# Kernel tuning notes

Hardware: AMD Instinct MI355X
Metric: run time of the kernel (lower is better)

## Reference

```python
import jax, jax.numpy as jnp
from jax import lax
import numpy as np

U = 512          # LSTMOutUnits
NL = 3           # stacked LSTM cells
EMB = 300
VOCAB = 50000
LABELS = 7
BN_EPS = 1e-3    # keras BatchNormalization default epsilon


def _lstm_cell(x, h, c, W, Uw, b):
    # keras LSTMCell: gates ordered i, f, g(c), o; activation=softsign, recurrent_activation=sigmoid
    z = x @ W + h @ Uw + b                      # [B, 4U]
    i, f, g, o = jnp.split(z, 4, axis=-1)
    c = jax.nn.sigmoid(f) * c + jax.nn.sigmoid(i) * jax.nn.soft_sign(g)
    h = jax.nn.sigmoid(o) * jax.nn.soft_sign(c)
    return h, c


def _run_stack(x_tbd, Ws, Us, bs):
    # x_tbd: [T, B, D]; returns final hidden state of top cell: [B, U]
    B = x_tbd.shape[1]
    init = tuple((jnp.zeros((B, U), x_tbd.dtype), jnp.zeros((B, U), x_tbd.dtype)) for _ in range(NL))

    def step(carry, x):
        new = []
        inp = x
        for (h, c), W, Uw, b in zip(carry, Ws, Us, bs):
            h, c = _lstm_cell(inp, h, c, W, Uw, b)
            new.append((h, c))
            inp = h
        return tuple(new), None

    carry, _ = lax.scan(step, init, x_tbd)
    return carry[-1][0]


def setup_inputs() -> dict:
    key = jax.random.key(0)
    ks = iter(jax.random.split(key, 40))
    d = {}
    d['ids'] = jax.random.randint(next(ks), (128, 128), 0, VOCAB, dtype=jnp.int32)
    d['emb'] = jax.random.normal(next(ks), (VOCAB, EMB), jnp.float32)
    for pre in ('f', 'b'):
        for l in range(NL):
            din = EMB if l == 0 else U
            d[f'{pre}W{l}'] = jax.random.normal(next(ks), (din, 4 * U), jnp.float32) * 0.05
            d[f'{pre}U{l}'] = jax.random.normal(next(ks), (U, 4 * U), jnp.float32) * 0.05
            d[f'{pre}b{l}'] = jnp.zeros((4 * U,), jnp.float32)
    d['d0_W'] = jax.random.normal(next(ks), (U, U // 2), jnp.float32) * 0.05
    d['d0_b'] = jnp.zeros((U // 2,), jnp.float32)
    d['bn_gamma'] = jnp.ones((U // 2,), jnp.float32)
    d['bn_beta'] = jnp.zeros((U // 2,), jnp.float32)
    d['bn_mean'] = jnp.zeros((U // 2,), jnp.float32)
    d['bn_var'] = jnp.ones((U // 2,), jnp.float32)
    d['prelu_alpha'] = jnp.full((U // 2,), 0.25, jnp.float32)
    d['d1_W'] = jax.random.normal(next(ks), (U // 2, LABELS), jnp.float32) * 0.05
    d['d1_b'] = jnp.zeros((LABELS,), jnp.float32)
    return d


def reference(ids, emb,
              fW0, fU0, fb0, fW1, fU1, fb1, fW2, fU2, fb2,
              bW0, bU0, bb0, bW1, bU1, bb1, bW2, bU2, bb2,
              d0_W, d0_b, bn_gamma, bn_beta, bn_mean, bn_var,
              prelu_alpha, d1_W, d1_b):
    x = lax.stop_gradient(jnp.take(emb, ids, axis=0))      # [B, T, EMB]
    x = jnp.transpose(x, (1, 0, 2))                        # [T, B, EMB]
    fwd = _run_stack(x, (fW0, fW1, fW2), (fU0, fU1, fU2), (fb0, fb1, fb2))
    bwd = _run_stack(x[::-1], (bW0, bW1, bW2), (bU0, bU1, bU2), (bb0, bb1, bb2))
    add = 0.5 * (fwd + bwd)                                # [B, U]
    h = add @ d0_W + d0_b                                  # [B, U//2]
    h = (h - bn_mean) * lax.rsqrt(bn_var + BN_EPS) * bn_gamma + bn_beta
    h = jnp.where(h > 0, h, prelu_alpha * h)               # PReLU
    logits = h @ d1_W + d1_b                               # [B, LABELS]
    return jax.nn.softmax(logits, axis=-1)
```

## Files before the change

kernel.cpp:

```cpp
#include <hip/hip_runtime.h>
#include <hip/hip_bf16.h>
#include <math.h>

#define TT   128
#define BB   128
#define UU   512
#define EMBD 300
#define EMBP 320
#define NBLK 192
#define DBLK 96
#define NTHR 512
#define BSTR 1032

using bf16x8 = __attribute__((ext_vector_type(8))) short;
using f32x4  = __attribute__((ext_vector_type(4))) float;

#define NEED_WS 111681536ull
static void* g_pool = nullptr;
__attribute__((constructor)) static void alloc_pool() {
    if (hipMalloc(&g_pool, 120ull * 1024ull * 1024ull) != hipSuccess) g_pool = nullptr;
}

__device__ __forceinline__ float b2f(unsigned short u) {
    union { unsigned int i; float f; } v; v.i = ((unsigned int)u) << 16; return v.f;
}
__device__ __forceinline__ unsigned short f2b(float f) {
    union { unsigned int i; float f; } v; v.f = f;
    unsigned int i = v.i;
    return (unsigned short)((i + 0x7fffu + ((i >> 16) & 1u)) >> 16);
}
__device__ __forceinline__ unsigned short ld_bf(const void* p, size_t i, int f32) {
    return f32 ? f2b(((const float*)p)[i]) : ((const unsigned short*)p)[i];
}
__device__ __forceinline__ float ld_f(const void* p, size_t i, int f32) {
    return f32 ? ((const float*)p)[i] : b2f(((const unsigned short*)p)[i]);
}
__device__ __forceinline__ float clampz(float x) {
    return fminf(fmaxf(x, -60.0f), 60.0f);
}
__device__ __forceinline__ float sigm(float x)  { return 1.0f / (1.0f + __expf(-x)); }
__device__ __forceinline__ float ssign(float x) { return x / (1.0f + fabsf(x)); }

__device__ __forceinline__ int detect_f32(const void* emb) {
    const unsigned int* w = (const unsigned int*)emb;
    int cnt = 0;
    #pragma unroll
    for (int i = 0; i < 64; ++i) {
        unsigned int e = (w[i] >> 23) & 0xFFu;
        cnt += (e >= 96u && e <= 159u) ? 1 : 0;
    }
    return cnt >= 48;
}

struct P {
    const int* ids;
    const void* emb;
    const void* Wm[2][3];
    const void* Um[2][3];
    const void* bm[2][3];
    const void *d0W, *d0b;
    const void *bn_gamma, *bn_beta, *bn_mean, *bn_var;
    const void *alpha, *d1W, *d1b;
    unsigned short* X;
    unsigned short* H;
    float* hf;
    unsigned int* flags;
    unsigned int* epoch;
    float* out;
};

#define EPOFF 64

__device__ __forceinline__ unsigned int ald(const unsigned int* a) {
    return __hip_atomic_load(a, __ATOMIC_RELAXED, __HIP_MEMORY_SCOPE_AGENT);
}
__device__ __forceinline__ void ast(unsigned int* a, unsigned int v) {
    __hip_atomic_store(a, v, __ATOMIC_RELAXED, __HIP_MEMORY_SCOPE_AGENT);
}

__device__ __forceinline__ void gsync_fence(unsigned int* flags, unsigned int gen) {
    __syncthreads();
    if (threadIdx.x == 0) {
        __threadfence();
        ast(&flags[blockIdx.x], gen);
    }
    if (threadIdx.x < 64) {
        const int i = threadIdx.x;
        for (;;) {
            bool ok = true;
            #pragma unroll
            for (int j = 0; j < NBLK / 64; ++j)
                ok = ok && (ald(&flags[i + j * 64]) >= gen);
            if (__all(ok)) break;
            __builtin_amdgcn_s_sleep(1);
        }
        __threadfence();
    }
    __syncthreads();
}

__device__ __forceinline__ void gsync_dir(P& p, int dirbase, int eidx, int isagg, unsigned int gen) {
    __syncthreads();
    if (threadIdx.x == 0)
        ast(&p.flags[blockIdx.x], gen);
    if (isagg && threadIdx.x < 64) {
        const unsigned int* f = p.flags + dirbase + threadIdx.x;
        const bool two = (threadIdx.x < DBLK - 64);
        for (;;) {
            bool ok = (ald(f) >= gen) && (!two || (ald(f + 64) >= gen));
            if (__all(ok)) break;
            __builtin_amdgcn_s_sleep(1);
        }
        if (threadIdx.x == 0)
            ast(&p.epoch[eidx], gen);
    }
    if (threadIdx.x < 64) {
        const unsigned int* e = &p.epoch[eidx];
        while (ald(e) < gen) __builtin_amdgcn_s_sleep(1);
    }
    __syncthreads();
}

__device__ __forceinline__ void gsync_all(P& p, int dirbase, int eidx, int isagg, unsigned int gen) {
    __syncthreads();
    if (threadIdx.x == 0)
        ast(&p.flags[blockIdx.x], gen);
    if (isagg && threadIdx.x < 64) {
        const unsigned int* f = p.flags + dirbase + threadIdx.x;
        const bool two = (threadIdx.x < DBLK - 64);
        for (;;) {
            bool ok = (ald(f) >= gen) && (!two || (ald(f + 64) >= gen));
            if (__all(ok)) break;
            __builtin_amdgcn_s_sleep(1);
        }
        if (threadIdx.x == 0)
            ast(&p.epoch[eidx], gen);
    }
    if (threadIdx.x < 64) {
        while (!((ald(&p.epoch[0]) >= gen) && (ald(&p.epoch[EPOFF]) >= gen)))
            __builtin_amdgcn_s_sleep(1);
    }
    __syncthreads();
}

template<int K1T, int BOFF>
__device__ __forceinline__ void mfma_part(
    const unsigned short* __restrict__ a0p,
    const unsigned short* __restrict__ bp,
    f32x4 (&acc)[4])
{
    #pragma unroll 4
    for (int kt = 0; kt < K1T; kt += 32) {
        bf16x8 av = *(const bf16x8*)(a0p + kt);
        #pragma unroll
        for (int ct = 0; ct < 4; ++ct) {
            bf16x8 bv = *(const bf16x8*)(bp + (size_t)ct * 16 * BSTR + BOFF + kt);
            acc[ct] = __builtin_amdgcn_mfma_f32_16x16x32_bf16(av, bv, acc[ct], 0, 0, 0);
        }
    }
}

__global__ __launch_bounds__(NTHR, 1) void bilstm_persistent(P p) {
    const int blk = blockIdx.x;
    const int tid = threadIdx.x;

    const int f32 = detect_f32(p.emb);
    unsigned int gen = 0;

    __shared__ __align__(16) unsigned short Bt[64][BSTR];
    __shared__ __align__(16) float zbuf[8][2][16][17];
    __shared__ float hact[256];
    __shared__ float lgts[8];

    for (int row = blk; row < TT * BB; row += NBLK) {
        int t = row >> 7, b = row & 127;
        int id = p.ids[b * TT + t];
        unsigned short* xr = p.X + (size_t)row * EMBP;
        for (int k2 = tid; k2 < EMBP; k2 += NTHR)
            xr[k2] = (k2 < EMBD) ? ld_bf(p.emb, (size_t)id * EMBD + k2, f32)
                                 : (unsigned short)0;
    }
    gsync_fence(p.flags, ++gen);

    const int dir     = (blk >= DBLK) ? 1 : 0;
    const int rb      = blk - dir * DBLK;
    const int layer   = rb >> 5;
    const int dirbase = dir * DBLK;
    const int eidx    = dir * EPOFF;
    const int isagg   = (rb == 0);
    const int j0      = (rb & 31) * 16;

    const int wv   = tid >> 6;
    const int lane = tid & 63;
    const int l15  = lane & 15;
    const int quad = lane >> 4;

    const int row16 = lane & 15;
    const int jp    = (lane >> 4) & 1;
    const int ch    = lane >> 5;

    const int r0   = wv * 16 + l15;
    const int ko   = quad * 8;

    float cS[2][2];
    cS[0][0] = cS[0][1] = cS[1][0] = cS[1][1] = 0.0f;

    const size_t seq = (size_t)TT * BB * UU;

    const int KW   = (layer == 0) ? EMBD : UU;
    const int K1   = (layer == 0) ? EMBP : UU;
    const int Ktot = K1 + UU;
    const void* Wmat = p.Wm[dir][layer];
    const void* Umat = p.Um[dir][layer];
    const void* bias = p.bm[dir][layer];
    {
        int n = tid >> 3, ks = tid & 7;
        int wcol = ((n >> 2) & 3) * UU + j0 + (n >> 4) * 4 + (n & 3);
        for (int k2 = ks; k2 < Ktot; k2 += 8) {
            unsigned short v;
            if (k2 < KW)      v = ld_bf(Wmat, (size_t)k2 * 2048 + wcol, f32);
            else if (k2 < K1) v = 0;
            else              v = ld_bf(Umat, (size_t)(k2 - K1) * 2048 + wcol, f32);
            Bt[n][k2] = v;
        }
    }
    float bz[2][4][2];
    #pragma unroll
    for (int pp = 0; pp < 2; ++pp) {
        const int cb = j0 + (2 * pp + ch) * 4 + 2 * jp;
        #pragma unroll
        for (int g = 0; g < 4; ++g) {
            bz[pp][g][0] = ld_f(bias, g * UU + cb,     f32);
            bz[pp][g][1] = ld_f(bias, g * UU + cb + 1, f32);
        }
    }
    __syncthreads();

    unsigned short*       Hl  = p.H + (size_t)(layer * 2 + dir) * seq;
    const unsigned short* Hin = (layer > 0) ? (p.H + (size_t)((layer - 1) * 2 + dir) * seq) : nullptr;

    const unsigned short* bp = &Bt[l15][ko];
    float* zbw = &zbuf[wv][0][0][0];

    for (int s = 0; s < TT + 2; ++s) {
        const int t = s - layer;
        if (t >= 0 && t < TT) {
            const unsigned short* A2 = (t > 0) ? (Hl + (size_t)(t - 1) * BB * UU) : nullptr;

            f32x4 acc[4];
            #pragma unroll
            for (int ct = 0; ct < 4; ++ct) acc[ct] = f32x4{0.f, 0.f, 0.f, 0.f};

            if (layer == 0) {
                int tx = dir ? (TT - 1 - t) : t;
                const unsigned short* A1 = p.X + (size_t)tx * BB * EMBP;
                mfma_part<EMBP, 0>(A1 + (size_t)r0 * EMBP + ko, bp, acc);
                if (A2)
                    mfma_part<UU, EMBP>(A2 + (size_t)r0 * UU + ko, bp, acc);
            } else {
                const unsigned short* A1 = Hin + (size_t)t * BB * UU;
                mfma_part<UU, 0>(A1 + (size_t)r0 * UU + ko, bp, acc);
                if (A2)
                    mfma_part<UU, UU>(A2 + (size_t)r0 * UU + ko, bp, acc);
            }

            #pragma unroll
            for (int pp = 0; pp < 2; ++pp) {
                #pragma unroll
                for (int cth = 0; cth < 2; ++cth) {
                    const int ct = pp * 2 + cth;
                    #pragma unroll
                    for (int r = 0; r < 4; ++r)
                        zbw[cth * 272 + (quad * 4 + r) * 17 + l15] = acc[ct][r];
                }
                const int zb0 = ch * 272 + row16 * 17 + 2 * jp;
                float ziA = clampz(zbw[zb0 +  0] + bz[pp][0][0]);
                float zfA = clampz(zbw[zb0 +  4] + bz[pp][1][0]);
                float zgA = clampz(zbw[zb0 +  8] + bz[pp][2][0]);
                float zoA = clampz(zbw[zb0 + 12] + bz[pp][3][0]);
                float ziB = clampz(zbw[zb0 +  1] + bz[pp][0][1]);
                float zfB = clampz(zbw[zb0 +  5] + bz[pp][1][1]);
                float zgB = clampz(zbw[zb0 +  9] + bz[pp][2][1]);
                float zoB = clampz(zbw[zb0 + 13] + bz[pp][3][1]);
                float cpA = (t == 0) ? 0.0f : cS[pp][0];
                float cpB = (t == 0) ? 0.0f : cS[pp][1];
                float cnA = sigm(zfA) * cpA + sigm(ziA) * ssign(zgA);
                float cnB = sigm(zfB) * cpB + sigm(ziB) * ssign(zgB);
                cS[pp][0] = cnA; cS[pp][1] = cnB;
                float hA = sigm(zoA) * ssign(cnA);
                float hB = sigm(zoB) * ssign(cnB);
                const int R   = wv * 16 + row16;
                const int col = j0 + (2 * pp + ch) * 4 + 2 * jp;
                unsigned int pk = (unsigned int)f2b(hA) | ((unsigned int)f2b(hB) << 16);
                __hip_atomic_store((unsigned int*)&Hl[(size_t)t * BB * UU + (size_t)R * UU + col],
                                   pk, __ATOMIC_RELAXED, __HIP_MEMORY_SCOPE_AGENT);
                if (layer == 2 && t == TT - 1) {
                    size_t o = (size_t)dir * BB * UU + (size_t)R * UU + col;
                    __hip_atomic_store(&p.hf[o],     hA, __ATOMIC_RELAXED, __HIP_MEMORY_SCOPE_AGENT);
                    __hip_atomic_store(&p.hf[o + 1], hB, __ATOMIC_RELAXED, __HIP_MEMORY_SCOPE_AGENT);
                }
            }
        }
        gsync_dir(p, dirbase, eidx, isagg, ++gen);
    }

    gsync_all(p, dirbase, eidx, isagg, ++gen);

    if (blk < BB) {
        const int b = blk;
        if (tid < 256) {
            const float* h0 = p.hf + (size_t)b * UU;
            const float* h1 = p.hf + (size_t)BB * UU + (size_t)b * UU;
            float acc = ld_f(p.d0b, tid, f32);
            #pragma unroll 8
            for (int k = 0; k < UU; ++k) {
                float a = 0.5f * (h0[k] + h1[k]);
                acc = fmaf(a, ld_f(p.d0W, (size_t)k * 256 + tid, f32), acc);
            }
            acc = fminf(fmaxf(acc, -1e6f), 1e6f);
            float x = (acc - ld_f(p.bn_mean, tid, f32))
                      * rsqrtf(fmaxf(ld_f(p.bn_var, tid, f32), 0.0f) + 1e-3f)
                      * ld_f(p.bn_gamma, tid, f32) + ld_f(p.bn_beta, tid, f32);
            float al = ld_f(p.alpha, tid, f32);
            hact[tid] = (x > 0.f) ? x : al * x;
        }
        __syncthreads();
        if (tid < 7) {
            float s = ld_f(p.d1b, tid, f32);
            #pragma unroll 8
            for (int k = 0; k < 256; ++k)
                s = fmaf(hact[k], ld_f(p.d1W, k * 7 + tid, f32), s);
            lgts[tid] = fminf(fmaxf(s, -1e6f), 1e6f);
        }
        __syncthreads();
        if (tid == 0) {
            float mx = lgts[0];
            for (int j = 1; j < 7; ++j) mx = fmaxf(mx, lgts[j]);
            float ex[7]; float sum = 0.f;
            for (int j = 0; j < 7; ++j) { ex[j] = __expf(lgts[j] - mx); sum += ex[j]; }
            float inv = 1.0f / sum;
            for (int j = 0; j < 7; ++j) p.out[b * 7 + j] = ex[j] * inv;
        }
    }
}

extern "C" void kernel_launch(void* const* d_in, const int* in_sizes, int n_in,
                              void* d_out, int out_size, void* d_ws, size_t ws_size,
                              hipStream_t stream) {
    (void)in_sizes; (void)n_in; (void)out_size;

    P p;
    p.ids = (const int*)d_in[0];
    p.emb = d_in[1];
    for (int l = 0; l < 3; ++l) {
        p.Wm[0][l] = d_in[2 + l * 3];
        p.Um[0][l] = d_in[3 + l * 3];
        p.bm[0][l] = d_in[4 + l * 3];
        p.Wm[1][l] = d_in[11 + l * 3];
        p.Um[1][l] = d_in[12 + l * 3];
        p.bm[1][l] = d_in[13 + l * 3];
    }
    p.d0W      = d_in[20];
    p.d0b      = d_in[21];
    p.bn_gamma = d_in[22];
    p.bn_beta  = d_in[23];
    p.bn_mean  = d_in[24];
    p.bn_var   = d_in[25];
    p.alpha    = d_in[26];
    p.d1W      = d_in[27];
    p.d1b      = d_in[28];

    char* base = (ws_size >= NEED_WS || g_pool == nullptr) ? (char*)d_ws : (char*)g_pool;
    const size_t OFF_X  = 8192;
    const size_t OFF_H  = OFF_X + (size_t)TT * BB * EMBP * 2;
    const size_t OFF_HF = OFF_H + (size_t)3 * 2 * TT * BB * UU * 2;
    p.flags = (unsigned int*)base;
    p.epoch = (unsigned int*)(base + 4096);
    p.X     = (unsigned short*)(base + OFF_X);
    p.H     = (unsigned short*)(base + OFF_H);
    p.hf    = (float*)(base + OFF_HF);
    p.out   = (float*)d_out;

    hipMemsetAsync(base, 0, 8192, stream);
    hipLaunchKernelGGL(bilstm_persistent, dim3(NBLK), dim3(NTHR), 0, stream, p);
}
```

Baseline: 1.674 ms.

## Keep recurrent weights in registers and split K across waves

```diff
diff --git a/kernel.cpp b/kernel.cpp
--- a/kernel.cpp
+++ b/kernel.cpp
@@ -10,7 +10,7 @@
 #define NBLK 192
 #define DBLK 96
 #define NTHR 512
-#define BSTR 1032
+#define BTS  1032
 
 using bf16x8 = __attribute__((ext_vector_type(8))) short;
 using f32x4  = __attribute__((ext_vector_type(4))) float;
@@ -143,34 +143,20 @@
     __syncthreads();
 }
 
-template<int K1T, int BOFF>
-__device__ __forceinline__ void mfma_part(
-    const unsigned short* __restrict__ a0p,
-    const unsigned short* __restrict__ bp,
-    f32x4 (&acc)[4])
-{
-    #pragma unroll 4
-    for (int kt = 0; kt < K1T; kt += 32) {
-        bf16x8 av = *(const bf16x8*)(a0p + kt);
-        #pragma unroll
-        for (int ct = 0; ct < 4; ++ct) {
-            bf16x8 bv = *(const bf16x8*)(bp + (size_t)ct * 16 * BSTR + BOFF + kt);
-            acc[ct] = __builtin_amdgcn_mfma_f32_16x16x32_bf16(av, bv, acc[ct], 0, 0, 0);
-        }
-    }
-}
-
-__global__ __launch_bounds__(NTHR, 1) void bilstm_persistent(P p) {
+#define ZSTR 260
+
+__global__ __launch_bounds__(NTHR, 2) void bilstm_persistent(P p) {
     const int blk = blockIdx.x;
     const int tid = threadIdx.x;
 
     const int f32 = detect_f32(p.emb);
     unsigned int gen = 0;
 
-    __shared__ __align__(16) unsigned short Bt[64][BSTR];
-    __shared__ __align__(16) float zbuf[8][2][16][17];
+    __shared__ __align__(16) float smem[128 * ZSTR];
     __shared__ float hact[256];
     __shared__ float lgts[8];
+    unsigned short* Bt = (unsigned short*)smem;
+    float* zpart = smem;
 
     for (int row = blk; row < TT * BB; row += NBLK) {
         int t = row >> 7, b = row & 127;
@@ -194,111 +180,148 @@
     const int lane = tid & 63;
     const int l15  = lane & 15;
     const int quad = lane >> 4;
-
-    const int row16 = lane & 15;
-    const int jp    = (lane >> 4) & 1;
-    const int ch    = lane >> 5;
-
-    const int r0   = wv * 16 + l15;
     const int ko   = quad * 8;
 
-    float cS[2][2];
-    cS[0][0] = cS[0][1] = cS[1][0] = cS[1][1] = 0.0f;
+    const int kq   = wv & 3;
+    const int mh   = wv >> 2;
+
+    const int gr   = tid & 127;
+    const int ct4  = tid >> 7;
+
+    float cS[4] = {0.f, 0.f, 0.f, 0.f};
 
     const size_t seq = (size_t)TT * BB * UU;
 
-    const int KW   = (layer == 0) ? EMBD : UU;
-    const int K1   = (layer == 0) ? EMBP : UU;
-    const int Ktot = K1 + UU;
+    const int KW = (layer == 0) ? EMBD : UU;
     const void* Wmat = p.Wm[dir][layer];
     const void* Umat = p.Um[dir][layer];
     const void* bias = p.bm[dir][layer];
     {
         int n = tid >> 3, ks = tid & 7;
         int wcol = ((n >> 2) & 3) * UU + j0 + (n >> 4) * 4 + (n & 3);
-        for (int k2 = ks; k2 < Ktot; k2 += 8) {
+        for (int k2 = ks; k2 < 1024; k2 += 8) {
             unsigned short v;
-            if (k2 < KW)      v = ld_bf(Wmat, (size_t)k2 * 2048 + wcol, f32);
-            else if (k2 < K1) v = 0;
-            else              v = ld_bf(Umat, (size_t)(k2 - K1) * 2048 + wcol, f32);
-            Bt[n][k2] = v;
-        }
-    }
-    float bz[2][4][2];
+            if (k2 < KW)        v = ld_bf(Wmat, (size_t)k2 * 2048 + wcol, f32);
+            else if (k2 < 512)  v = 0;
+            else                v = ld_bf(Umat, (size_t)(k2 - 512) * 2048 + wcol, f32);
+            Bt[n * BTS + k2] = v;
+        }
+    }
+    float bz[4][4];
     #pragma unroll
-    for (int pp = 0; pp < 2; ++pp) {
-        const int cb = j0 + (2 * pp + ch) * 4 + 2 * jp;
+    for (int g = 0; g < 4; ++g)
         #pragma unroll
-        for (int g = 0; g < 4; ++g) {
-            bz[pp][g][0] = ld_f(bias, g * UU + cb,     f32);
-            bz[pp][g][1] = ld_f(bias, g * UU + cb + 1, f32);
-        }
-    }
-    __syncthreads();
+        for (int jj = 0; jj < 4; ++jj)
+            bz[g][jj] = ld_f(bias, g * UU + j0 + ct4 * 4 + jj, f32);
+    __syncthreads();
+
+    bf16x8 breg[8][4];
+    #pragma unroll
+    for (int kt = 0; kt < 8; ++kt)
+        #pragma unroll
+        for (int ct = 0; ct < 4; ++ct)
+            breg[kt][ct] = *(const bf16x8*)&Bt[(ct * 16 + l15) * BTS + (kq * 8 + kt) * 32 + ko];
+    __syncthreads();
+
+    int koff[8];
+    if (kq < 2) {
+        if (layer == 0) {
+            #pragma unroll
+            for (int kt = 0; kt < 8; ++kt) {
+                int tk = kq * 8 + kt;
+                koff[kt] = (tk < 10) ? tk * 32 : 0;
+            }
+        } else {
+            #pragma unroll
+            for (int kt = 0; kt < 8; ++kt) koff[kt] = kq * 256 + kt * 32;
+        }
+    } else {
+        #pragma unroll
+        for (int kt = 0; kt < 8; ++kt) koff[kt] = (kq - 2) * 256 + kt * 32;
+    }
 
     unsigned short*       Hl  = p.H + (size_t)(layer * 2 + dir) * seq;
     const unsigned short* Hin = (layer > 0) ? (p.H + (size_t)((layer - 1) * 2 + dir) * seq) : nullptr;
 
-    const unsigned short* bp = &Bt[l15][ko];
-    float* zbw = &zbuf[wv][0][0][0];
-
     for (int s = 0; s < TT + 2; ++s) {
         const int t = s - layer;
-        if (t >= 0 && t < TT) {
-            const unsigned short* A2 = (t > 0) ? (Hl + (size_t)(t - 1) * BB * UU) : nullptr;
-
-            f32x4 acc[4];
+        const bool tv = (t >= 0 && t < TT);
+
+        if (tv) {
+            const unsigned short* Abase = nullptr;
+            int astr = 0;
+            if (kq < 2) {
+                if (layer == 0) {
+                    int tx = dir ? (TT - 1 - t) : t;
+                    Abase = p.X + (size_t)tx * BB * EMBP;  astr = EMBP;
+                } else {
+                    Abase = Hin + (size_t)t * BB * UU;     astr = UU;
+                }
+            } else if (t > 0) {
+                Abase = Hl + (size_t)(t - 1) * BB * UU;    astr = UU;
+            }
+            if (Abase) {
+                #pragma unroll
+                for (int rt = 0; rt < 4; ++rt) {
+                    const unsigned short* ap =
+                        Abase + (size_t)(mh * 64 + rt * 16 + l15) * astr + ko;
+                    bf16x8 av[8];
+                    #pragma unroll
+                    for (int kt = 0; kt < 8; ++kt)
+                        av[kt] = *(const bf16x8*)(ap + koff[kt]);
+                    f32x4 acc[4];
+                    #pragma unroll
+                    for (int ct = 0; ct < 4; ++ct) acc[ct] = f32x4{0.f, 0.f, 0.f, 0.f};
+                    #pragma unroll
+                    for (int kt = 0; kt < 8; ++kt)
+                        #pragma unroll
+                        for (int ct = 0; ct < 4; ++ct)
+                            acc[ct] = __builtin_amdgcn_mfma_f32_16x16x32_bf16(
+                                av[kt], breg[kt][ct], acc[ct], 0, 0, 0);
+                    const int rbase = mh * 64 + rt * 16 + quad * 4;
+                    #pragma unroll
+                    for (int ct = 0; ct < 4; ++ct)
+                        #pragma unroll
+                        for (int rg = 0; rg < 4; ++rg)
+                            zpart[(rbase + rg) * ZSTR + (ct * 16 + l15) * 4 + kq] = acc[ct][rg];
+                }
+            }
+        }
+        __syncthreads();
+
+        if (tv) {
+            float hv[4];
             #pragma unroll
-            for (int ct = 0; ct < 4; ++ct) acc[ct] = f32x4{0.f, 0.f, 0.f, 0.f};
-
-            if (layer == 0) {
-                int tx = dir ? (TT - 1 - t) : t;
-                const unsigned short* A1 = p.X + (size_t)tx * BB * EMBP;
-                mfma_part<EMBP, 0>(A1 + (size_t)r0 * EMBP + ko, bp, acc);
-                if (A2)
-                    mfma_part<UU, EMBP>(A2 + (size_t)r0 * UU + ko, bp, acc);
-            } else {
-                const unsigned short* A1 = Hin + (size_t)t * BB * UU;
-                mfma_part<UU, 0>(A1 + (size_t)r0 * UU + ko, bp, acc);
-                if (A2)
-                    mfma_part<UU, UU>(A2 + (size_t)r0 * UU + ko, bp, acc);
-            }
-
-            #pragma unroll
-            for (int pp = 0; pp < 2; ++pp) {
+            for (int jj = 0; jj < 4; ++jj) {
+                float z[4];
                 #pragma unroll
-                for (int cth = 0; cth < 2; ++cth) {
-                    const int ct = pp * 2 + cth;
-                    #pragma unroll
-                    for (int r = 0; r < 4; ++r)
-                        zbw[cth * 272 + (quad * 4 + r) * 17 + l15] = acc[ct][r];
+                for (int g = 0; g < 4; ++g) {
+                    const f32x4 v = *(const f32x4*)&zpart[gr * ZSTR + (ct4 * 16 + g * 4 + jj) * 4];
+                    float zz = v[0] + v[1];
+                    if (t > 0) zz += v[2] + v[3];
+                    z[g] = zz;
                 }
-                const int zb0 = ch * 272 + row16 * 17 + 2 * jp;
-                float ziA = clampz(zbw[zb0 +  0] + bz[pp][0][0]);
-                float zfA = clampz(zbw[zb0 +  4] + bz[pp][1][0]);
-                float zgA = clampz(zbw[zb0 +  8] + bz[pp][2][0]);
-                float zoA = clampz(zbw[zb0 + 12] + bz[pp][3][0]);
-                float ziB = clampz(zbw[zb0 +  1] + bz[pp][0][1]);
-                float zfB = clampz(zbw[zb0 +  5] + bz[pp][1][1]);
-                float zgB = clampz(zbw[zb0 +  9] + bz[pp][2][1]);
-                float zoB = clampz(zbw[zb0 + 13] + bz[pp][3][1]);
-                float cpA = (t == 0) ? 0.0f : cS[pp][0];
-                float cpB = (t == 0) ? 0.0f : cS[pp][1];
-                float cnA = sigm(zfA) * cpA + sigm(ziA) * ssign(zgA);
-                float cnB = sigm(zfB) * cpB + sigm(ziB) * ssign(zgB);
-                cS[pp][0] = cnA; cS[pp][1] = cnB;
-                float hA = sigm(zoA) * ssign(cnA);
-                float hB = sigm(zoB) * ssign(cnB);
-                const int R   = wv * 16 + row16;
-                const int col = j0 + (2 * pp + ch) * 4 + 2 * jp;
-                unsigned int pk = (unsigned int)f2b(hA) | ((unsigned int)f2b(hB) << 16);
-                __hip_atomic_store((unsigned int*)&Hl[(size_t)t * BB * UU + (size_t)R * UU + col],
-                                   pk, __ATOMIC_RELAXED, __HIP_MEMORY_SCOPE_AGENT);
-                if (layer == 2 && t == TT - 1) {
-                    size_t o = (size_t)dir * BB * UU + (size_t)R * UU + col;
-                    __hip_atomic_store(&p.hf[o],     hA, __ATOMIC_RELAXED, __HIP_MEMORY_SCOPE_AGENT);
-                    __hip_atomic_store(&p.hf[o + 1], hB, __ATOMIC_RELAXED, __HIP_MEMORY_SCOPE_AGENT);
-                }
+                float zi = clampz(z[0] + bz[0][jj]);
+                float zf = clampz(z[1] + bz[1][jj]);
+                float zg = clampz(z[2] + bz[2][jj]);
+                float zo = clampz(z[3] + bz[3][jj]);
+                float cp = (t == 0) ? 0.0f : cS[jj];
+                float cn = sigm(zf) * cp + sigm(zi) * ssign(zg);
+                cS[jj] = cn;
+                hv[jj] = sigm(zo) * ssign(cn);
+            }
+            const int col = j0 + ct4 * 4;
+            unsigned int pk0 = (unsigned int)f2b(hv[0]) | ((unsigned int)f2b(hv[1]) << 16);
+            unsigned int pk1 = (unsigned int)f2b(hv[2]) | ((unsigned int)f2b(hv[3]) << 16);
+            unsigned int* hp = (unsigned int*)&Hl[(size_t)t * BB * UU + (size_t)gr * UU + col];
+            __hip_atomic_store(hp,     pk0, __ATOMIC_RELAXED, __HIP_MEMORY_SCOPE_AGENT);
+            __hip_atomic_store(hp + 1, pk1, __ATOMIC_RELAXED, __HIP_MEMORY_SCOPE_AGENT);
+            if (layer == 2 && t == TT - 1) {
+                size_t o = (size_t)dir * BB * UU + (size_t)gr * UU + col;
+                #pragma unroll
+                for (int jj = 0; jj < 4; ++jj)
+                    __hip_atomic_store(&p.hf[o + jj], hv[jj],
+                                       __ATOMIC_RELAXED, __HIP_MEMORY_SCOPE_AGENT);
             }
         }
         gsync_dir(p, dirbase, eidx, isagg, ++gen);
```

Result: slower. 2.094 ms (+25.1%).

## Retile per-wave MFMA work to 2x2 blocks to share A and B fragments

Applied to the files above, without the earlier changes.

```diff
diff --git a/kernel.cpp b/kernel.cpp
--- a/kernel.cpp
+++ b/kernel.cpp
@@ -11,6 +11,7 @@
 #define DBLK 96
 #define NTHR 512
 #define BSTR 1032
+#define ZST  34
 
 using bf16x8 = __attribute__((ext_vector_type(8))) short;
 using f32x4  = __attribute__((ext_vector_type(4))) float;
@@ -146,17 +147,21 @@
 template<int K1T, int BOFF>
 __device__ __forceinline__ void mfma_part(
     const unsigned short* __restrict__ a0p,
-    const unsigned short* __restrict__ bp,
-    f32x4 (&acc)[4])
+    const unsigned short* __restrict__ a1p,
+    const unsigned short* __restrict__ bp0,
+    const unsigned short* __restrict__ bp1,
+    f32x4 (&acc)[2][2])
 {
     #pragma unroll 4
     for (int kt = 0; kt < K1T; kt += 32) {
-        bf16x8 av = *(const bf16x8*)(a0p + kt);
-        #pragma unroll
-        for (int ct = 0; ct < 4; ++ct) {
-            bf16x8 bv = *(const bf16x8*)(bp + (size_t)ct * 16 * BSTR + BOFF + kt);
-            acc[ct] = __builtin_amdgcn_mfma_f32_16x16x32_bf16(av, bv, acc[ct], 0, 0, 0);
-        }
+        bf16x8 av0 = *(const bf16x8*)(a0p + kt);
+        bf16x8 av1 = *(const bf16x8*)(a1p + kt);
+        bf16x8 bv0 = *(const bf16x8*)(bp0 + BOFF + kt);
+        bf16x8 bv1 = *(const bf16x8*)(bp1 + BOFF + kt);
+        acc[0][0] = __builtin_amdgcn_mfma_f32_16x16x32_bf16(av0, bv0, acc[0][0], 0, 0, 0);
+        acc[0][1] = __builtin_amdgcn_mfma_f32_16x16x32_bf16(av0, bv1, acc[0][1], 0, 0, 0);
+        acc[1][0] = __builtin_amdgcn_mfma_f32_16x16x32_bf16(av1, bv0, acc[1][0], 0, 0, 0);
+        acc[1][1] = __builtin_amdgcn_mfma_f32_16x16x32_bf16(av1, bv1, acc[1][1], 0, 0, 0);
     }
 }
 
@@ -168,7 +173,7 @@
     unsigned int gen = 0;
 
     __shared__ __align__(16) unsigned short Bt[64][BSTR];
-    __shared__ __align__(16) float zbuf[8][2][16][17];
+    __shared__ __align__(16) float zbuf[8][16 * ZST];
     __shared__ float hact[256];
     __shared__ float lgts[8];
 
@@ -194,13 +199,13 @@
     const int lane = tid & 63;
     const int l15  = lane & 15;
     const int quad = lane >> 4;
-
-    const int row16 = lane & 15;
-    const int jp    = (lane >> 4) & 1;
-    const int ch    = lane >> 5;
-
-    const int r0   = wv * 16 + l15;
     const int ko   = quad * 8;
+
+    const int mt   = wv >> 1;
+    const int nh   = wv & 1;
+
+    const int crow = lane >> 2;
+    const int hc0  = (lane & 3) * 2;
 
     float cS[2][2];
     cS[0][0] = cS[0][1] = cS[1][0] = cS[1][1] = 0.0f;
@@ -215,7 +220,7 @@
     const void* bias = p.bm[dir][layer];
     {
         int n = tid >> 3, ks = tid & 7;
-        int wcol = ((n >> 2) & 3) * UU + j0 + (n >> 4) * 4 + (n & 3);
+        int wcol = ((n >> 3) & 3) * 512 + j0 + (n >> 5) * 8 + (n & 7);
         for (int k2 = ks; k2 < Ktot; k2 += 8) {
             unsigned short v;
             if (k2 < KW)      v = ld_bf(Wmat, (size_t)k2 * 2048 + wcol, f32);
@@ -224,80 +229,80 @@
             Bt[n][k2] = v;
         }
     }
-    float bz[2][4][2];
+    float bz[4][2];
     #pragma unroll
-    for (int pp = 0; pp < 2; ++pp) {
-        const int cb = j0 + (2 * pp + ch) * 4 + 2 * jp;
-        #pragma unroll
-        for (int g = 0; g < 4; ++g) {
-            bz[pp][g][0] = ld_f(bias, g * UU + cb,     f32);
-            bz[pp][g][1] = ld_f(bias, g * UU + cb + 1, f32);
-        }
+    for (int g = 0; g < 4; ++g) {
+        bz[g][0] = ld_f(bias, g * UU + j0 + nh * 8 + hc0,     f32);
+        bz[g][1] = ld_f(bias, g * UU + j0 + nh * 8 + hc0 + 1, f32);
     }
     __syncthreads();
 
     unsigned short*       Hl  = p.H + (size_t)(layer * 2 + dir) * seq;
     const unsigned short* Hin = (layer > 0) ? (p.H + (size_t)((layer - 1) * 2 + dir) * seq) : nullptr;
 
-    const unsigned short* bp = &Bt[l15][ko];
-    float* zbw = &zbuf[wv][0][0][0];
+    const unsigned short* bp0 = &Bt[nh * 32 + l15][ko];
+    const unsigned short* bp1 = &Bt[nh * 32 + 16 + l15][ko];
+    float* zbw = &zbuf[wv][0];
 
     for (int s = 0; s < TT + 2; ++s) {
         const int t = s - layer;
         if (t >= 0 && t < TT) {
             const unsigned short* A2 = (t > 0) ? (Hl + (size_t)(t - 1) * BB * UU) : nullptr;
 
-            f32x4 acc[4];
+            f32x4 acc[2][2];
             #pragma unroll
-            for (int ct = 0; ct < 4; ++ct) acc[ct] = f32x4{0.f, 0.f, 0.f, 0.f};
+            for (int a = 0; a < 2; ++a) {
+                acc[a][0] = f32x4{0.f, 0.f, 0.f, 0.f};
+                acc[a][1] = f32x4{0.f, 0.f, 0.f, 0.f};
+            }
 
             if (layer == 0) {
                 int tx = dir ? (TT - 1 - t) : t;
                 const unsigned short* A1 = p.X + (size_t)tx * BB * EMBP;
-                mfma_part<EMBP, 0>(A1 + (size_t)r0 * EMBP + ko, bp, acc);
-                if (A2)
-                    mfma_part<UU, EMBP>(A2 + (size_t)r0 * UU + ko, bp, acc);
+                const unsigned short* a0 = A1 + (size_t)(mt * 32 + l15) * EMBP + ko;
+                mfma_part<EMBP, 0>(a0, a0 + 16 * EMBP, bp0, bp1, acc);
+                if (A2) {
+                    const unsigned short* c0 = A2 + (size_t)(mt * 32 + l15) * UU + ko;
+                    mfma_part<UU, EMBP>(c0, c0 + 16 * UU, bp0, bp1, acc);
+                }
             } else {
                 const unsigned short* A1 = Hin + (size_t)t * BB * UU;
-                mfma_part<UU, 0>(A1 + (size_t)r0 * UU + ko, bp, acc);
-                if (A2)
-                    mfma_part<UU, UU>(A2 + (size_t)r0 * UU + ko, bp, acc);
+                const unsigned short* a0 = A1 + (size_t)(mt * 32 + l15) * UU + ko;
+                mfma_part<UU, 0>(a0, a0 + 16 * UU, bp0, bp1, acc);
+                if (A2) {
+                    const unsigned short* c0 = A2 + (size_t)(mt * 32 + l15) * UU + ko;
+                    mfma_part<UU, UU>(c0, c0 + 16 * UU, bp0, bp1, acc);
+                }
             }
 
             #pragma unroll
-            for (int pp = 0; pp < 2; ++pp) {
+            for (int a = 0; a < 2; ++a) {
                 #pragma unroll
-                for (int cth = 0; cth < 2; ++cth) {
-                    const int ct = pp * 2 + cth;
+                for (int b = 0; b < 2; ++b)
                     #pragma unroll
                     for (int r = 0; r < 4; ++r)
-                        zbw[cth * 272 + (quad * 4 + r) * 17 + l15] = acc[ct][r];
+                        zbw[(quad * 4 + r) * ZST + b * 16 + l15] = acc[a][b][r];
+                const int R = mt * 32 + a * 16 + crow;
+                float hv[2];
+                #pragma unroll
+                for (int hh = 0; hh < 2; ++hh) {
+                    float zi = clampz(zbw[crow * ZST +  0 + hc0 + hh] + bz[0][hh]);
+                    float zf = clampz(zbw[crow * ZST +  8 + hc0 + hh] + bz[1][hh]);
+                    float zg = clampz(zbw[crow * ZST + 16 + hc0 + hh] + bz[2][hh]);
+                    float zo = clampz(zbw[crow * ZST + 24 + hc0 + hh] + bz[3][hh]);
+                    float cp = (t == 0) ? 0.0f : cS[a][hh];
+                    float cn = sigm(zf) * cp + sigm(zi) * ssign(zg);
+                    cS[a][hh] = cn;
+                    hv[hh] = sigm(zo) * ssign(cn);
                 }
-                const int zb0 = ch * 272 + row16 * 17 + 2 * jp;
-                float ziA = clampz(zbw[zb0 +  0] + bz[pp][0][0]);
-                float zfA = clampz(zbw[zb0 +  4] + bz[pp][1][0]);
-                float zgA = clampz(zbw[zb0 +  8] + bz[pp][2][0]);
-                float zoA = clampz(zbw[zb0 + 12] + bz[pp][3][0]);
-                float ziB = clampz(zbw[zb0 +  1] + bz[pp][0][1]);
-                float zfB = clampz(zbw[zb0 +  5] + bz[pp][1][1]);
-                float zgB = clampz(zbw[zb0 +  9] + bz[pp][2][1]);
-                float zoB = clampz(zbw[zb0 + 13] + bz[pp][3][1]);
-                float cpA = (t == 0) ? 0.0f : cS[pp][0];
-                float cpB = (t == 0) ? 0.0f : cS[pp][1];
-                float cnA = sigm(zfA) * cpA + sigm(ziA) * ssign(zgA);
-                float cnB = sigm(zfB) * cpB + sigm(ziB) * ssign(zgB);
-                cS[pp][0] = cnA; cS[pp][1] = cnB;
-                float hA = sigm(zoA) * ssign(cnA);
-                float hB = sigm(zoB) * ssign(cnB);
-                const int R   = wv * 16 + row16;
-                const int col = j0 + (2 * pp + ch) * 4 + 2 * jp;
-                unsigned int pk = (unsigned int)f2b(hA) | ((unsigned int)f2b(hB) << 16);
+                const int col = j0 + nh * 8 + hc0;
+                unsigned int pk = (unsigned int)f2b(hv[0]) | ((unsigned int)f2b(hv[1]) << 16);
                 __hip_atomic_store((unsigned int*)&Hl[(size_t)t * BB * UU + (size_t)R * UU + col],
                                    pk, __ATOMIC_RELAXED, __HIP_MEMORY_SCOPE_AGENT);
                 if (layer == 2 && t == TT - 1) {
                     size_t o = (size_t)dir * BB * UU + (size_t)R * UU + col;
-                    __hip_atomic_store(&p.hf[o],     hA, __ATOMIC_RELAXED, __HIP_MEMORY_SCOPE_AGENT);
-                    __hip_atomic_store(&p.hf[o + 1], hB, __ATOMIC_RELAXED, __HIP_MEMORY_SCOPE_AGENT);
+                    __hip_atomic_store(&p.hf[o],     hv[0], __ATOMIC_RELAXED, __HIP_MEMORY_SCOPE_AGENT);
+                    __hip_atomic_store(&p.hf[o + 1], hv[1], __ATOMIC_RELAXED, __HIP_MEMORY_SCOPE_AGENT);
                 }
             }
         }
```

Result: slower. 2.571 ms (+53.6%).

## Replace per-direction grid barrier with per-layer dependency epochs and prefetch A operands

Applied to the files above, without the earlier changes.

```diff
diff --git a/kernel.cpp b/kernel.cpp
--- a/kernel.cpp
+++ b/kernel.cpp
@@ -69,8 +69,6 @@
     float* out;
 };
 
-#define EPOFF 64
-
 __device__ __forceinline__ unsigned int ald(const unsigned int* a) {
     return __hip_atomic_load(a, __ATOMIC_RELAXED, __HIP_MEMORY_SCOPE_AGENT);
 }
@@ -99,73 +97,47 @@
     __syncthreads();
 }
 
-__device__ __forceinline__ void gsync_dir(P& p, int dirbase, int eidx, int isagg, unsigned int gen) {
-    __syncthreads();
-    if (threadIdx.x == 0)
-        ast(&p.flags[blockIdx.x], gen);
-    if (isagg && threadIdx.x < 64) {
-        const unsigned int* f = p.flags + dirbase + threadIdx.x;
-        const bool two = (threadIdx.x < DBLK - 64);
-        for (;;) {
-            bool ok = (ald(f) >= gen) && (!two || (ald(f + 64) >= gen));
-            if (__all(ok)) break;
-            __builtin_amdgcn_s_sleep(1);
-        }
-        if (threadIdx.x == 0)
-            ast(&p.epoch[eidx], gen);
-    }
-    if (threadIdx.x < 64) {
-        const unsigned int* e = &p.epoch[eidx];
-        while (ald(e) < gen) __builtin_amdgcn_s_sleep(1);
-    }
-    __syncthreads();
-}
-
-__device__ __forceinline__ void gsync_all(P& p, int dirbase, int eidx, int isagg, unsigned int gen) {
-    __syncthreads();
-    if (threadIdx.x == 0)
-        ast(&p.flags[blockIdx.x], gen);
-    if (isagg && threadIdx.x < 64) {
-        const unsigned int* f = p.flags + dirbase + threadIdx.x;
-        const bool two = (threadIdx.x < DBLK - 64);
-        for (;;) {
-            bool ok = (ald(f) >= gen) && (!two || (ald(f + 64) >= gen));
-            if (__all(ok)) break;
-            __builtin_amdgcn_s_sleep(1);
-        }
-        if (threadIdx.x == 0)
-            ast(&p.epoch[eidx], gen);
-    }
-    if (threadIdx.x < 64) {
-        while (!((ald(&p.epoch[0]) >= gen) && (ald(&p.epoch[EPOFF]) >= gen)))
-            __builtin_amdgcn_s_sleep(1);
-    }
-    __syncthreads();
-}
-
-template<int K1T, int BOFF>
-__device__ __forceinline__ void mfma_part(
-    const unsigned short* __restrict__ a0p,
+template<int K1T>
+__device__ __forceinline__ void mfma_all(
+    const unsigned short* __restrict__ a1p,
+    const unsigned short* __restrict__ a2p,
     const unsigned short* __restrict__ bp,
     f32x4 (&acc)[4])
 {
-    #pragma unroll 4
-    for (int kt = 0; kt < K1T; kt += 32) {
-        bf16x8 av = *(const bf16x8*)(a0p + kt);
+    constexpr int N1 = K1T / 32;
+    bf16x8 av1[N1];
+    #pragma unroll
+    for (int i = 0; i < N1; ++i) av1[i] = *(const bf16x8*)(a1p + i * 32);
+    bf16x8 av2[16];
+    if (a2p) {
+        #pragma unroll
+        for (int i = 0; i < 16; ++i) av2[i] = *(const bf16x8*)(a2p + i * 32);
+    }
+    #pragma unroll
+    for (int i = 0; i < N1; ++i) {
         #pragma unroll
         for (int ct = 0; ct < 4; ++ct) {
-            bf16x8 bv = *(const bf16x8*)(bp + (size_t)ct * 16 * BSTR + BOFF + kt);
-            acc[ct] = __builtin_amdgcn_mfma_f32_16x16x32_bf16(av, bv, acc[ct], 0, 0, 0);
-        }
-    }
-}
-
-__global__ __launch_bounds__(NTHR, 1) void bilstm_persistent(P p) {
+            bf16x8 bv = *(const bf16x8*)(bp + (size_t)ct * 16 * BSTR + i * 32);
+            acc[ct] = __builtin_amdgcn_mfma_f32_16x16x32_bf16(av1[i], bv, acc[ct], 0, 0, 0);
+        }
+    }
+    if (a2p) {
+        #pragma unroll
+        for (int i = 0; i < 16; ++i) {
+            #pragma unroll
+            for (int ct = 0; ct < 4; ++ct) {
+                bf16x8 bv = *(const bf16x8*)(bp + (size_t)ct * 16 * BSTR + K1T + i * 32);
+                acc[ct] = __builtin_amdgcn_mfma_f32_16x16x32_bf16(av2[i], bv, acc[ct], 0, 0, 0);
+            }
+        }
+    }
+}
+
+__global__ __launch_bounds__(NTHR, 2) void bilstm_persistent(P p) {
     const int blk = blockIdx.x;
     const int tid = threadIdx.x;
 
     const int f32 = detect_f32(p.emb);
-    unsigned int gen = 0;
 
     __shared__ __align__(16) unsigned short Bt[64][BSTR];
     __shared__ __align__(16) float zbuf[8][2][16][17];
@@ -180,14 +152,15 @@
             xr[k2] = (k2 < EMBD) ? ld_bf(p.emb, (size_t)id * EMBD + k2, f32)
                                  : (unsigned short)0;
     }
-    gsync_fence(p.flags, ++gen);
+    gsync_fence(p.flags, 1u);
 
     const int dir     = (blk >= DBLK) ? 1 : 0;
     const int rb      = blk - dir * DBLK;
     const int layer   = rb >> 5;
     const int dirbase = dir * DBLK;
-    const int eidx    = dir * EPOFF;
-    const int isagg   = (rb == 0);
+    const int isagg   = ((rb & 31) == 0);
+    const int eL      = (dir * 3 + layer) * 64;
+    const int eLm1    = eL - 64;
     const int j0      = (rb & 31) * 16;
 
     const int wv   = tid >> 6;
@@ -244,8 +217,33 @@
 
     for (int s = 0; s < TT + 2; ++s) {
         const int t = s - layer;
-        if (t >= 0 && t < TT) {
-            const unsigned short* A2 = (t > 0) ? (Hl + (size_t)(t - 1) * BB * UU) : nullptr;
+        const bool tv = (t >= 0 && t < TT);
+
+        if (tv && s > 0) {
+            const unsigned int need = (unsigned int)(s + 1);
+            if (tid < 64) {
+                if (layer == 0) {
+                    if (t > 0) {
+                        const unsigned int* e = &p.epoch[eL];
+                        while (ald(e) < need) __builtin_amdgcn_s_sleep(1);
+                    }
+                } else {
+                    const unsigned int* ein = &p.epoch[eLm1];
+                    if (t > 0) {
+                        const unsigned int* eo = &p.epoch[eL];
+                        while (!((ald(ein) >= need) && (ald(eo) >= need)))
+                            __builtin_amdgcn_s_sleep(1);
+                    } else {
+                        while (ald(ein) < need) __builtin_amdgcn_s_sleep(1);
+                    }
+                }
+            }
+            __syncthreads();
+        }
+
+        if (tv) {
+            const unsigned short* A2r = (t > 0)
+                ? (Hl + (size_t)(t - 1) * BB * UU + (size_t)r0 * UU + ko) : nullptr;
 
             f32x4 acc[4];
             #pragma unroll
@@ -254,14 +252,10 @@
             if (layer == 0) {
                 int tx = dir ? (TT - 1 - t) : t;
                 const unsigned short* A1 = p.X + (size_t)tx * BB * EMBP;
-                mfma_part<EMBP, 0>(A1 + (size_t)r0 * EMBP + ko, bp, acc);
-                if (A2)
-                    mfma_part<UU, EMBP>(A2 + (size_t)r0 * UU + ko, bp, acc);
+                mfma_all<EMBP>(A1 + (size_t)r0 * EMBP + ko, A2r, bp, acc);
             } else {
                 const unsigned short* A1 = Hin + (size_t)t * BB * UU;
-                mfma_part<UU, 0>(A1 + (size_t)r0 * UU + ko, bp, acc);
-                if (A2)
-                    mfma_part<UU, UU>(A2 + (size_t)r0 * UU + ko, bp, acc);
+                mfma_all<UU>(A1 + (size_t)r0 * UU + ko, A2r, bp, acc);
             }
 
             #pragma unroll
@@ -301,10 +295,21 @@
                 }
             }
         }
-        gsync_dir(p, dirbase, eidx, isagg, ++gen);
-    }
-
-    gsync_all(p, dirbase, eidx, isagg, ++gen);
+
+        __syncthreads();
+        if (tid == 0) ast(&p.flags[blk], (unsigned int)(s + 2));
+
+        if (isagg) {
+            const unsigned int g = (unsigned int)(s + 2);
+            if (tid < 64) {
+                const unsigned int* f = p.flags + dirbase + layer * 32 + (tid & 31);
+                while (!__all(ald(f) >= g)) __builtin_amdgcn_s_sleep(1);
+            }
+            if (tid == 0) ast(&p.epoch[eL], g);
+        }
+    }
+
+    gsync_fence(p.flags, (unsigned int)(TT + 4));
 
     if (blk < BB) {
         const int b = blk;
```

Result: slower. 1.965 ms (+17.4%).
